# Kernel optimization log

Measured on AMD Instinct MI355X. Metric: run time of the kernel, lower is better.

## Reference

```python
import jax, jax.numpy as jnp
import numpy as np

N_TOKENS = 65536   # number of embeddings to quantize
CODE_DIM = 768     # embedding dim
NUM_CODES = 4096   # codebook size


def setup_inputs() -> dict:
    key = jax.random.key(0)
    k1, k2 = jax.random.split(key)
    x = jax.random.normal(k1, (N_TOKENS, CODE_DIM), dtype=jnp.float32)
    codebook = jax.random.normal(k2, (NUM_CODES, CODE_DIM), dtype=jnp.float32)
    return {"x": x, "codebook": codebook}


def reference(x, codebook):
    # argmin over squared distances == argmin over cdist (sqrt is monotone).
    x2 = jnp.sum(x * x, axis=-1, keepdims=True)          # [N, 1]
    c2 = jnp.sum(codebook * codebook, axis=-1)           # [K]
    dist = x2 + c2[None, :] - 2.0 * jnp.einsum('nd,kd->nk', x, codebook)  # [N, K]
    indices = jnp.argmin(dist, axis=-1)                  # [N] int
    quantized = codebook[indices]                        # gather [N, D]
    # straight-through estimator: forward = quantized, grad flows to x
    q_ste = x + jax.lax.stop_gradient(quantized - x)
    return q_ste, indices
```

## Files before the change

kernel.cpp:

```cpp
#include <hip/hip_runtime.h>

#define N_TOKENS  65536
#define CODE_DIM  768
#define NUM_CODES 4096

#define MARGIN 0.006f
#define FLTMAX 3.4028235e38f

typedef __attribute__((ext_vector_type(8))) short bf16x8;
typedef __attribute__((ext_vector_type(4))) float f32x4;

__device__ __forceinline__ unsigned short f2bf(float f) {
  unsigned int u = __float_as_uint(f);
  unsigned int r = (u + 0x7fffu + ((u >> 16) & 1u)) >> 16;
  return (unsigned short)r;
}
__device__ __forceinline__ float bf2f(unsigned short h) {
  return __uint_as_float(((unsigned int)h) << 16);
}
__device__ __forceinline__ void gl2lds16(const void* g, void* l) {
  __builtin_amdgcn_global_load_lds(
      (const __attribute__((address_space(1))) unsigned int*)g,
      (__attribute__((address_space(3))) unsigned int*)l, 16, 0, 0);
}

__global__ __launch_bounds__(256) void vq_convert_kernel(
    const float* __restrict__ x, const float* __restrict__ cb,
    unsigned short* __restrict__ xh, unsigned short* __restrict__ xl,
    unsigned short* __restrict__ cbh, unsigned short* __restrict__ cbl,
    float* __restrict__ x2, float* __restrict__ c2, int* __restrict__ fcnt) {
  if (blockIdx.x == 0 && threadIdx.x == 0) *fcnt = 0;
  const int wave = threadIdx.x >> 6;
  const int lane = threadIdx.x & 63;
  const int row  = blockIdx.x * 4 + wave;
  const float* src;
  unsigned short *hdst, *ldst;
  float* ndst;
  if (row < N_TOKENS) {
    src = x + (size_t)row * CODE_DIM;
    hdst = xh + (size_t)row * CODE_DIM;
    ldst = xl + (size_t)row * CODE_DIM;
    ndst = x2 + row;
  } else {
    const int r = row - N_TOKENS;
    if (r >= NUM_CODES) return;
    src = cb + (size_t)r * CODE_DIM;
    hdst = cbh + (size_t)r * CODE_DIM;
    ldst = cbl + (size_t)r * CODE_DIM;
    ndst = c2 + r;
  }
  const float4* s4 = (const float4*)src;
  ushort4* h4 = (ushort4*)hdst;
  ushort4* l4 = (ushort4*)ldst;
  float acc = 0.f;
#pragma unroll
  for (int i = 0; i < 3; ++i) {
    float4 f = s4[lane + 64 * i];
    ushort4 h, l;
    h.x = f2bf(f.x); l.x = f2bf(f.x - bf2f(h.x));
    h.y = f2bf(f.y); l.y = f2bf(f.y - bf2f(h.y));
    h.z = f2bf(f.z); l.z = f2bf(f.z - bf2f(h.z));
    h.w = f2bf(f.w); l.w = f2bf(f.w - bf2f(h.w));
    h4[lane + 64 * i] = h;
    l4[lane + 64 * i] = l;
    acc += (f.x * f.x + f.y * f.y) + (f.z * f.z + f.w * f.w);
  }
#pragma unroll
  for (int off = 32; off > 0; off >>= 1) acc += __shfl_down(acc, off, 64);
  if (lane == 0) *ndst = acc;
}

#define BT 256
#define KTILE 256
#define NKT (NUM_CODES / KTILE)
#define NSTEP (CODE_DIM / 32)
#define TOTSTEP (NKT * NSTEP)

__global__ __launch_bounds__(512, 2) void vq_mfma_kernel(
    const unsigned short* __restrict__ xh, const unsigned short* __restrict__ xl,
    const unsigned short* __restrict__ cbh, const unsigned short* __restrict__ cbl,
    const float* __restrict__ c2, const float* __restrict__ cb,
    float* __restrict__ out, int* __restrict__ out_idx,
    int* __restrict__ fcnt, int* __restrict__ flist) {
  __shared__ __align__(16) unsigned short sA[2][BT * 64];
  __shared__ __align__(16) unsigned short sB[2][KTILE * 64];
  __shared__ float redv[512], redsv[512];
  __shared__ int   redi[512];
  __shared__ int   sIdx[256];

  const int tid = threadIdx.x;
  const int wave = tid >> 6, lane = tid & 63;
  const int l15 = lane & 15, quad = lane >> 4;
  const int wr = wave >> 1, wc = wave & 1;
  const int tokBase = blockIdx.x * BT;

  const int lr = lane >> 3;
  const int cc = (lane & 7) ^ lr;
  const int hsel = cc >> 2;
  const int coff = (cc & 3) * 8;
  const unsigned short* pAsrc = hsel ? xl : xh;
  const unsigned short* pBsrc = hsel ? cbl : cbh;
  const size_t aOff = (size_t)(tokBase + wave * 32 + lr) * CODE_DIM + coff;
  const size_t bOff = (size_t)(wave * 32 + lr) * CODE_DIM + coff;

  const int aposh = (quad ^ (l15 & 7)) * 8;
  const int aBaseH = (wr * 64 + l15) * 64 + aposh;
  const int aBaseL = (wr * 64 + l15) * 64 + (aposh ^ 32);
  const int bBaseH = (wc * 128 + l15) * 64 + aposh;
  const int bBaseL = (wc * 128 + l15) * 64 + (aposh ^ 32);

  float v[4][4], sv[4][4];
  int bi[4][4];
#pragma unroll
  for (int i = 0; i < 4; ++i)
#pragma unroll
    for (int r = 0; r < 4; ++r) { v[i][r] = FLTMAX; sv[i][r] = FLTMAX; bi[i][r] = 0; }

  {
#pragma unroll
    for (int t = 0; t < 4; ++t)
      gl2lds16(pAsrc + aOff + (size_t)t * (8 * CODE_DIM),
               &sA[0][(wave * 32 + t * 8) * 64]);
#pragma unroll
    for (int t = 0; t < 4; ++t)
      gl2lds16(pBsrc + bOff + (size_t)t * (8 * CODE_DIM),
               &sB[0][(wave * 32 + t * 8) * 64]);
  }
  asm volatile("s_waitcnt vmcnt(0)" ::: "memory");
  __builtin_amdgcn_s_barrier();
  __builtin_amdgcn_sched_barrier(0);

  for (int kt = 0; kt < NKT; ++kt) {
    f32x4 acc[4][8];
#pragma unroll
    for (int i = 0; i < 4; ++i)
#pragma unroll
      for (int j = 0; j < 8; ++j) acc[i][j] = (f32x4){0.f, 0.f, 0.f, 0.f};

    for (int ksq = 0; ksq < NSTEP; ++ksq) {
      const int gstep = kt * NSTEP + ksq;
      const int cur = gstep & 1;
      const bool more = (gstep < TOTSTEP - 1);
      const int ns = gstep + 1;
      const int nk0 = (ns % NSTEP) * 32;
      const size_t nbb = (size_t)(ns / NSTEP) * (KTILE * (size_t)CODE_DIM);
      const unsigned short* As = sA[cur];
      const unsigned short* Bs = sB[cur];

      if (more) {
#pragma unroll
        for (int t = 0; t < 4; ++t)
          gl2lds16(pAsrc + aOff + (size_t)t * (8 * CODE_DIM) + nk0,
                   &sA[cur ^ 1][(wave * 32 + t * 8) * 64]);
      }

      bf16x8 fah[4], fal[4], fbh[8], fbl[8];
#pragma unroll
      for (int i = 0; i < 4; ++i) fah[i] = *(const bf16x8*)(As + aBaseH + i * 1024);
#pragma unroll
      for (int j = 0; j < 8; ++j) fbh[j] = *(const bf16x8*)(Bs + bBaseH + j * 1024);
      __builtin_amdgcn_s_setprio(1);
#pragma unroll
      for (int i = 0; i < 4; ++i)
#pragma unroll
        for (int j = 0; j < 8; ++j)
          acc[i][j] = __builtin_amdgcn_mfma_f32_16x16x32_bf16(fah[i], fbh[j], acc[i][j], 0, 0, 0);
      __builtin_amdgcn_s_setprio(0);

      if (more) {
#pragma unroll
        for (int t = 0; t < 4; ++t)
          gl2lds16(pBsrc + nbb + bOff + (size_t)t * (8 * CODE_DIM) + nk0,
                   &sB[cur ^ 1][(wave * 32 + t * 8) * 64]);
      }

#pragma unroll
      for (int j = 0; j < 8; ++j) fbl[j] = *(const bf16x8*)(Bs + bBaseL + j * 1024);
      __builtin_amdgcn_s_setprio(1);
#pragma unroll
      for (int i = 0; i < 4; ++i)
#pragma unroll
        for (int j = 0; j < 8; ++j)
          acc[i][j] = __builtin_amdgcn_mfma_f32_16x16x32_bf16(fah[i], fbl[j], acc[i][j], 0, 0, 0);
      __builtin_amdgcn_s_setprio(0);

#pragma unroll
      for (int i = 0; i < 4; ++i) fal[i] = *(const bf16x8*)(As + aBaseL + i * 1024);
      __builtin_amdgcn_s_setprio(1);
#pragma unroll
      for (int i = 0; i < 4; ++i)
#pragma unroll
        for (int j = 0; j < 8; ++j)
          acc[i][j] = __builtin_amdgcn_mfma_f32_16x16x32_bf16(fal[i], fbh[j], acc[i][j], 0, 0, 0);
      __builtin_amdgcn_s_setprio(0);

      asm volatile("s_waitcnt vmcnt(0)" ::: "memory");
      __builtin_amdgcn_s_barrier();
      __builtin_amdgcn_sched_barrier(0);
    }

    const int kbase = kt * KTILE;
#pragma unroll
    for (int j = 0; j < 8; ++j) {
      const int kcol = kbase + wc * 128 + j * 16 + l15;
      const float c2j = c2[kcol];
#pragma unroll
      for (int i = 0; i < 4; ++i)
#pragma unroll
        for (int r = 0; r < 4; ++r) {
          float s = fmaf(-2.0f, acc[i][j][r], c2j);
          float vo = v[i][r];
          sv[i][r] = fminf(sv[i][r], fmaxf(s, vo));
          bool lt = s < vo;
          v[i][r]  = lt ? s : vo;
          bi[i][r] = lt ? kcol : bi[i][r];
        }
    }
  }

#pragma unroll
  for (int i = 0; i < 4; ++i)
#pragma unroll
    for (int r = 0; r < 4; ++r) {
      float vv = v[i][r], svv = sv[i][r];
      int ii = bi[i][r];
#pragma unroll
      for (int m = 1; m < 16; m <<= 1) {
        float ov = __shfl_xor(vv, m, 64);
        float osv = __shfl_xor(svv, m, 64);
        int oi = __shfl_xor(ii, m, 64);
        float nsv = fminf(fminf(svv, osv), fmaxf(vv, ov));
        bool take = (ov < vv) || (ov == vv && oi < ii);
        vv = take ? ov : vv;
        ii = take ? oi : ii;
        svv = nsv;
      }
      if (l15 == 0) {
        int row = wr * 64 + i * 16 + quad * 4 + r;
        redv[row * 2 + wc] = vv;
        redsv[row * 2 + wc] = svv;
        redi[row * 2 + wc] = ii;
      }
    }
  __syncthreads();
  if (tid < 256) {
    float v0 = redv[tid * 2], v1 = redv[tid * 2 + 1];
    float s0 = redsv[tid * 2], s1 = redsv[tid * 2 + 1];
    int i0 = redi[tid * 2], i1 = redi[tid * 2 + 1];
    bool take = (v1 < v0) || (v1 == v0 && i1 < i0);
    float bv = take ? v1 : v0;
    int bidx = take ? i1 : i0;
    float bsv = fminf(fminf(s0, s1), fmaxf(v0, v1));
    out_idx[tokBase + tid] = bidx;
    sIdx[tid] = bidx;
    if (bsv - bv < MARGIN) {
      int p = atomicAdd(fcnt, 1);
      flist[p] = tokBase + tid;
    }
  }
  __syncthreads();
  for (int tt = 0; tt < 32; ++tt) {
    const int t = wave * 32 + tt;
    const int k = sIdx[t];
    const float4* src = (const float4*)(cb + (size_t)k * CODE_DIM);
    float4* dst = (float4*)(out + (size_t)(tokBase + t) * CODE_DIM);
#pragma unroll
    for (int i2 = 0; i2 < 3; ++i2) dst[lane + 64 * i2] = src[lane + 64 * i2];
  }
  if (tid < 256)
    out[(size_t)N_TOKENS * CODE_DIM + tokBase + tid] = (float)sIdx[tid];
}

__global__ __launch_bounds__(256) void vq_rescan_kernel(
    const float* __restrict__ x, const float* __restrict__ cb,
    const float* __restrict__ x2, const float* __restrict__ c2,
    const int* __restrict__ fcnt, const int* __restrict__ flist,
    int* __restrict__ out_idx, float* __restrict__ out) {
  __shared__ float xs[4][CODE_DIM];
  __shared__ float rv[256];
  __shared__ int ri[256];
  const int nf = *fcnt;
  const int ngr = (nf + 3) >> 2;
  for (int g = blockIdx.x; g < ngr; g += gridDim.x) {
    const int base = g * 4;
    int tok[4];
#pragma unroll
    for (int t = 0; t < 4; ++t) tok[t] = flist[min(base + t, nf - 1)];
    __syncthreads();
    if (threadIdx.x < 192) {
#pragma unroll
      for (int t = 0; t < 4; ++t)
        ((float4*)xs[t])[threadIdx.x] =
            ((const float4*)(x + (size_t)tok[t] * CODE_DIM))[threadIdx.x];
    }
    __syncthreads();
    float bv[4]; int bidx[4];
#pragma unroll
    for (int t = 0; t < 4; ++t) { bv[t] = FLTMAX; bidx[t] = 0; }
    for (int kk = 0; kk < NUM_CODES / 256; ++kk) {
      const int k = kk * 256 + threadIdx.x;
      const float4* crow = (const float4*)(cb + (size_t)k * CODE_DIM);
      float a0 = 0.f, a1 = 0.f, a2 = 0.f, a3 = 0.f;
      for (int c = 0; c < CODE_DIM / 4; ++c) {
        float4 cv = crow[c];
        float4 x0 = ((float4*)xs[0])[c];
        float4 x1 = ((float4*)xs[1])[c];
        float4 x2v = ((float4*)xs[2])[c];
        float4 x3 = ((float4*)xs[3])[c];
        a0 += (x0.x * cv.x + x0.y * cv.y) + (x0.z * cv.z + x0.w * cv.w);
        a1 += (x1.x * cv.x + x1.y * cv.y) + (x1.z * cv.z + x1.w * cv.w);
        a2 += (x2v.x * cv.x + x2v.y * cv.y) + (x2v.z * cv.z + x2v.w * cv.w);
        a3 += (x3.x * cv.x + x3.y * cv.y) + (x3.z * cv.z + x3.w * cv.w);
      }
      const float c2k = c2[k];
      float d0 = (x2[tok[0]] + c2k) - 2.0f * a0;
      float d1 = (x2[tok[1]] + c2k) - 2.0f * a1;
      float d2 = (x2[tok[2]] + c2k) - 2.0f * a2;
      float d3 = (x2[tok[3]] + c2k) - 2.0f * a3;
      if (d0 < bv[0]) { bv[0] = d0; bidx[0] = k; }
      if (d1 < bv[1]) { bv[1] = d1; bidx[1] = k; }
      if (d2 < bv[2]) { bv[2] = d2; bidx[2] = k; }
      if (d3 < bv[3]) { bv[3] = d3; bidx[3] = k; }
    }
#pragma unroll
    for (int t = 0; t < 4; ++t) {
      __syncthreads();
      rv[threadIdx.x] = bv[t];
      ri[threadIdx.x] = bidx[t];
      __syncthreads();
      for (int s = 128; s > 0; s >>= 1) {
        if (threadIdx.x < s) {
          float ov = rv[threadIdx.x + s];
          int oi = ri[threadIdx.x + s];
          if (ov < rv[threadIdx.x] ||
              (ov == rv[threadIdx.x] && oi < ri[threadIdx.x])) {
            rv[threadIdx.x] = ov;
            ri[threadIdx.x] = oi;
          }
        }
        __syncthreads();
      }
      const int kfix = ri[0];
      if (base + t < nf) {
        if (threadIdx.x < 192)
          ((float4*)(out + (size_t)tok[t] * CODE_DIM))[threadIdx.x] =
              ((const float4*)(cb + (size_t)kfix * CODE_DIM))[threadIdx.x];
        if (threadIdx.x == 0) {
          out_idx[tok[t]] = kfix;
          out[(size_t)N_TOKENS * CODE_DIM + tok[t]] = (float)kfix;
        }
      }
    }
  }
}

__global__ __launch_bounds__(256) void vq_gather_kernel(
    const float* __restrict__ cb, const int* __restrict__ idx,
    float* __restrict__ out) {
  const int wave = threadIdx.x >> 6;
  const int lane = threadIdx.x & 63;
  const int token = blockIdx.x * 4 + wave;
  const int k = idx[token];
  const float4* src = (const float4*)(cb + (size_t)k * CODE_DIM);
  float4* dst = (float4*)(out + (size_t)token * CODE_DIM);
#pragma unroll
  for (int i = 0; i < 3; ++i) dst[lane + 64 * i] = src[lane + 64 * i];
  if (lane == 0) out[(size_t)N_TOKENS * CODE_DIM + token] = (float)k;
}

#define MT 64
#define KT 128
#define DT 32
#define LDSTRIDE 36

__global__ __launch_bounds__(256) void vq_norms_kernel(
    const float* __restrict__ x, const float* __restrict__ cb,
    float* __restrict__ x2, float* __restrict__ c2) {
  const int wave = threadIdx.x >> 6;
  const int lane = threadIdx.x & 63;
  const int row = blockIdx.x * 4 + wave;
  const float* src;
  float* dst;
  if (row < N_TOKENS) {
    src = x + (size_t)row * CODE_DIM;
    dst = x2 + row;
  } else {
    const int r = row - N_TOKENS;
    if (r >= NUM_CODES) return;
    src = cb + (size_t)r * CODE_DIM;
    dst = c2 + r;
  }
  const float4* s4 = (const float4*)src;
  float acc = 0.f;
#pragma unroll
  for (int i = 0; i < 3; ++i) {
    float4 vv = s4[lane + 64 * i];
    acc += (vv.x * vv.x + vv.y * vv.y) + (vv.z * vv.z + vv.w * vv.w);
  }
#pragma unroll
  for (int off = 32; off > 0; off >>= 1) acc += __shfl_down(acc, off, 64);
  if (lane == 0) *dst = acc;
}

__global__ __launch_bounds__(256) void vq_argmin_kernel(
    const float* __restrict__ x, const float* __restrict__ cb,
    const float* __restrict__ x2, const float* __restrict__ c2,
    int* __restrict__ out_idx) {
  __shared__ float xs[MT * LDSTRIDE];
  __shared__ float cs[KT * LDSTRIDE];
  __shared__ float x2s[MT];
  __shared__ float c2s[KT];
  const int tid = threadIdx.x;
  const int tx = tid & 15;
  const int ty = tid >> 4;
  const int tokBase = blockIdx.x * MT;
  if (tid < MT) x2s[tid] = x2[tokBase + tid];
  float bestv[4];
  int besti[4];
#pragma unroll
  for (int i = 0; i < 4; ++i) { bestv[i] = FLTMAX; besti[i] = 0; }
  const float4* xg = (const float4*)x;
  const float4* cg = (const float4*)cb;
  for (int kt = 0; kt < NUM_CODES / KT; ++kt) {
    const int kBase = kt * KT;
    __syncthreads();
    if (tid < KT) c2s[tid] = c2[kBase + tid];
    float acc[4][8];
#pragma unroll
    for (int i = 0; i < 4; ++i)
#pragma unroll
      for (int j = 0; j < 8; ++j) acc[i][j] = 0.f;
    for (int dc = 0; dc < CODE_DIM / DT; ++dc) {
      __syncthreads();
#pragma unroll
      for (int r = 0; r < 2; ++r) {
        int fidx = tid + 256 * r;
        int row = fidx >> 3, c4 = fidx & 7;
        float4 vv = xg[(size_t)(tokBase + row) * (CODE_DIM / 4) + dc * 8 + c4];
        *(float4*)&xs[row * LDSTRIDE + c4 * 4] = vv;
      }
#pragma unroll
      for (int r = 0; r < 4; ++r) {
        int fidx = tid + 256 * r;
        int row = fidx >> 3, c4 = fidx & 7;
        float4 vv = cg[(size_t)(kBase + row) * (CODE_DIM / 4) + dc * 8 + c4];
        *(float4*)&cs[row * LDSTRIDE + c4 * 4] = vv;
      }
      __syncthreads();
#pragma unroll
      for (int dd = 0; dd < DT / 4; ++dd) {
        float4 xv[4], cv[8];
#pragma unroll
        for (int i = 0; i < 4; ++i)
          xv[i] = *(const float4*)&xs[(ty + 16 * i) * LDSTRIDE + dd * 4];
#pragma unroll
        for (int j = 0; j < 8; ++j)
          cv[j] = *(const float4*)&cs[(tx + 16 * j) * LDSTRIDE + dd * 4];
#pragma unroll
        for (int i = 0; i < 4; ++i)
#pragma unroll
          for (int j = 0; j < 8; ++j)
            acc[i][j] += (xv[i].x * cv[j].x + xv[i].y * cv[j].y) +
                         (xv[i].z * cv[j].z + xv[i].w * cv[j].w);
      }
    }
#pragma unroll
    for (int i = 0; i < 4; ++i) {
      const float xx = x2s[ty + 16 * i];
#pragma unroll
      for (int j = 0; j < 8; ++j) {
        float dist = (xx + c2s[tx + 16 * j]) - 2.0f * acc[i][j];
        int k = kBase + tx + 16 * j;
        if (dist < bestv[i]) { bestv[i] = dist; besti[i] = k; }
      }
    }
  }
  __syncthreads();
  float* rdv = xs;
  int* rdi = (int*)cs;
#pragma unroll
  for (int i = 0; i < 4; ++i) {
    const int m = ty + 16 * i;
    rdv[m * 16 + tx] = bestv[i];
    rdi[m * 16 + tx] = besti[i];
  }
  __syncthreads();
  if (tid < MT) {
    float bv = rdv[tid * 16];
    int bidx = rdi[tid * 16];
#pragma unroll
    for (int t = 1; t < 16; ++t) {
      float vv = rdv[tid * 16 + t];
      int kk = rdi[tid * 16 + t];
      if (vv < bv || (vv == bv && kk < bidx)) { bv = vv; bidx = kk; }
    }
    out_idx[tokBase + tid] = bidx;
  }
}

extern "C" void kernel_launch(void* const* d_in, const int* in_sizes, int n_in,
                              void* d_out, int out_size, void* d_ws, size_t ws_size,
                              hipStream_t stream) {
  (void)in_sizes; (void)n_in; (void)out_size;
  const float* x = (const float*)d_in[0];
  const float* cb = (const float*)d_in[1];
  float* out = (float*)d_out;

  char* w = (char*)d_ws;
  unsigned short* xh = (unsigned short*)w;  w += (size_t)N_TOKENS * CODE_DIM * 2;
  unsigned short* xl = (unsigned short*)w;  w += (size_t)N_TOKENS * CODE_DIM * 2;
  unsigned short* cbh = (unsigned short*)w; w += (size_t)NUM_CODES * CODE_DIM * 2;
  unsigned short* cbl = (unsigned short*)w; w += (size_t)NUM_CODES * CODE_DIM * 2;
  float* x2 = (float*)w;  w += (size_t)N_TOKENS * 4;
  float* c2 = (float*)w;  w += (size_t)NUM_CODES * 4;
  int* idx = (int*)w;     w += (size_t)N_TOKENS * 4;
  int* flist = (int*)w;   w += (size_t)N_TOKENS * 4;
  int* fcnt = (int*)w;    w += 256;
  const size_t need = (size_t)(w - (char*)d_ws);

  if (ws_size >= need) {
    vq_convert_kernel<<<(N_TOKENS + NUM_CODES) / 4, 256, 0, stream>>>(
        x, cb, xh, xl, cbh, cbl, x2, c2, fcnt);
    vq_mfma_kernel<<<N_TOKENS / BT, 512, 0, stream>>>(
        xh, xl, cbh, cbl, c2, cb, out, idx, fcnt, flist);
    vq_rescan_kernel<<<512, 256, 0, stream>>>(x, cb, x2, c2, fcnt, flist, idx, out);
  } else {
    float* fx2 = (float*)d_ws;
    float* fc2 = fx2 + N_TOKENS;
    int* fidx = (int*)(fc2 + NUM_CODES);
    vq_norms_kernel<<<(N_TOKENS + NUM_CODES + 3) / 4, 256, 0, stream>>>(x, cb, fx2, fc2);
    vq_argmin_kernel<<<N_TOKENS / MT, 256, 0, stream>>>(x, cb, fx2, fc2, fidx);
    vq_gather_kernel<<<N_TOKENS / 4, 256, 0, stream>>>(cb, fidx, out);
  }
}
```

Baseline: 1.934 ms.

## Shrink MFMA block tile to 128x128 and move gather to separate kernel

Halves the token and codebook tile sizes, so each block runs 256 threads (4 waves) with a 4x4 MFMA accumulator tile instead of 8 waves with 4x8, and launches twice as many blocks. The codebook-row gather and index-as-float output move out of the MFMA and rescan kernels into the existing standalone gather kernel, which runs after the rescan. LDS fragment loads for the next step are now issued before the global-to-LDS prefetch. The smaller tile lowers per-block LDS and register use and should help occupancy, but it reduces operand reuse per byte loaded and adds another kernel launch.

New measurement: 2.178 ms. 1.13x slower.

```diff
diff --git a/kernel.cpp b/kernel.cpp
--- a/kernel.cpp
+++ b/kernel.cpp
@@ -70,23 +70,21 @@
   if (lane == 0) *ndst = acc;
 }
 
-#define BT 256
-#define KTILE 256
+#define BT 128
+#define KTILE 128
 #define NKT (NUM_CODES / KTILE)
 #define NSTEP (CODE_DIM / 32)
 #define TOTSTEP (NKT * NSTEP)
 
-__global__ __launch_bounds__(512, 2) void vq_mfma_kernel(
+__global__ __launch_bounds__(256, 2) void vq_mfma_kernel(
     const unsigned short* __restrict__ xh, const unsigned short* __restrict__ xl,
     const unsigned short* __restrict__ cbh, const unsigned short* __restrict__ cbl,
-    const float* __restrict__ c2, const float* __restrict__ cb,
-    float* __restrict__ out, int* __restrict__ out_idx,
+    const float* __restrict__ c2, int* __restrict__ out_idx,
     int* __restrict__ fcnt, int* __restrict__ flist) {
   __shared__ __align__(16) unsigned short sA[2][BT * 64];
   __shared__ __align__(16) unsigned short sB[2][KTILE * 64];
-  __shared__ float redv[512], redsv[512];
-  __shared__ int   redi[512];
-  __shared__ int   sIdx[256];
+  __shared__ float redv[256], redsv[256];
+  __shared__ int   redi[256];
 
   const int tid = threadIdx.x;
   const int wave = tid >> 6, lane = tid & 63;
@@ -106,8 +104,8 @@
   const int aposh = (quad ^ (l15 & 7)) * 8;
   const int aBaseH = (wr * 64 + l15) * 64 + aposh;
   const int aBaseL = (wr * 64 + l15) * 64 + (aposh ^ 32);
-  const int bBaseH = (wc * 128 + l15) * 64 + aposh;
-  const int bBaseL = (wc * 128 + l15) * 64 + (aposh ^ 32);
+  const int bBaseH = (wc * 64 + l15) * 64 + aposh;
+  const int bBaseL = (wc * 64 + l15) * 64 + (aposh ^ 32);
 
   float v[4][4], sv[4][4];
   int bi[4][4];
@@ -131,11 +129,11 @@
   __builtin_amdgcn_sched_barrier(0);
 
   for (int kt = 0; kt < NKT; ++kt) {
-    f32x4 acc[4][8];
+    f32x4 acc[4][4];
 #pragma unroll
     for (int i = 0; i < 4; ++i)
 #pragma unroll
-      for (int j = 0; j < 8; ++j) acc[i][j] = (f32x4){0.f, 0.f, 0.f, 0.f};
+      for (int j = 0; j < 4; ++j) acc[i][j] = (f32x4){0.f, 0.f, 0.f, 0.f};
 
     for (int ksq = 0; ksq < NSTEP; ++ksq) {
       const int gstep = kt * NSTEP + ksq;
@@ -147,6 +145,12 @@
       const unsigned short* As = sA[cur];
       const unsigned short* Bs = sB[cur];
 
+      bf16x8 fah[4], fal[4], fbh[4], fbl[4];
+#pragma unroll
+      for (int i = 0; i < 4; ++i) fah[i] = *(const bf16x8*)(As + aBaseH + i * 1024);
+#pragma unroll
+      for (int j = 0; j < 4; ++j) fbh[j] = *(const bf16x8*)(Bs + bBaseH + j * 1024);
+
       if (more) {
 #pragma unroll
         for (int t = 0; t < 4; ++t)
@@ -154,16 +158,11 @@
                    &sA[cur ^ 1][(wave * 32 + t * 8) * 64]);
       }
 
-      bf16x8 fah[4], fal[4], fbh[8], fbl[8];
-#pragma unroll
-      for (int i = 0; i < 4; ++i) fah[i] = *(const bf16x8*)(As + aBaseH + i * 1024);
-#pragma unroll
-      for (int j = 0; j < 8; ++j) fbh[j] = *(const bf16x8*)(Bs + bBaseH + j * 1024);
       __builtin_amdgcn_s_setprio(1);
 #pragma unroll
       for (int i = 0; i < 4; ++i)
 #pragma unroll
-        for (int j = 0; j < 8; ++j)
+        for (int j = 0; j < 4; ++j)
           acc[i][j] = __builtin_amdgcn_mfma_f32_16x16x32_bf16(fah[i], fbh[j], acc[i][j], 0, 0, 0);
       __builtin_amdgcn_s_setprio(0);
 
@@ -175,12 +174,12 @@
       }
 
 #pragma unroll
-      for (int j = 0; j < 8; ++j) fbl[j] = *(const bf16x8*)(Bs + bBaseL + j * 1024);
+      for (int j = 0; j < 4; ++j) fbl[j] = *(const bf16x8*)(Bs + bBaseL + j * 1024);
       __builtin_amdgcn_s_setprio(1);
 #pragma unroll
       for (int i = 0; i < 4; ++i)
 #pragma unroll
-        for (int j = 0; j < 8; ++j)
+        for (int j = 0; j < 4; ++j)
           acc[i][j] = __builtin_amdgcn_mfma_f32_16x16x32_bf16(fah[i], fbl[j], acc[i][j], 0, 0, 0);
       __builtin_amdgcn_s_setprio(0);
 
@@ -190,7 +189,7 @@
 #pragma unroll
       for (int i = 0; i < 4; ++i)
 #pragma unroll
-        for (int j = 0; j < 8; ++j)
+        for (int j = 0; j < 4; ++j)
           acc[i][j] = __builtin_amdgcn_mfma_f32_16x16x32_bf16(fal[i], fbh[j], acc[i][j], 0, 0, 0);
       __builtin_amdgcn_s_setprio(0);
 
@@ -201,8 +200,8 @@
 
     const int kbase = kt * KTILE;
 #pragma unroll
-    for (int j = 0; j < 8; ++j) {
-      const int kcol = kbase + wc * 128 + j * 16 + l15;
+    for (int j = 0; j < 4; ++j) {
+      const int kcol = kbase + wc * 64 + j * 16 + l15;
       const float c2j = c2[kcol];
 #pragma unroll
       for (int i = 0; i < 4; ++i)
@@ -243,7 +242,7 @@
       }
     }
   __syncthreads();
-  if (tid < 256) {
+  if (tid < 128) {
     float v0 = redv[tid * 2], v1 = redv[tid * 2 + 1];
     float s0 = redsv[tid * 2], s1 = redsv[tid * 2 + 1];
     int i0 = redi[tid * 2], i1 = redi[tid * 2 + 1];
@@ -252,30 +251,18 @@
     int bidx = take ? i1 : i0;
     float bsv = fminf(fminf(s0, s1), fmaxf(v0, v1));
     out_idx[tokBase + tid] = bidx;
-    sIdx[tid] = bidx;
     if (bsv - bv < MARGIN) {
       int p = atomicAdd(fcnt, 1);
       flist[p] = tokBase + tid;
     }
   }
-  __syncthreads();
-  for (int tt = 0; tt < 32; ++tt) {
-    const int t = wave * 32 + tt;
-    const int k = sIdx[t];
-    const float4* src = (const float4*)(cb + (size_t)k * CODE_DIM);
-    float4* dst = (float4*)(out + (size_t)(tokBase + t) * CODE_DIM);
-#pragma unroll
-    for (int i2 = 0; i2 < 3; ++i2) dst[lane + 64 * i2] = src[lane + 64 * i2];
-  }
-  if (tid < 256)
-    out[(size_t)N_TOKENS * CODE_DIM + tokBase + tid] = (float)sIdx[tid];
 }
 
 __global__ __launch_bounds__(256) void vq_rescan_kernel(
     const float* __restrict__ x, const float* __restrict__ cb,
     const float* __restrict__ x2, const float* __restrict__ c2,
     const int* __restrict__ fcnt, const int* __restrict__ flist,
-    int* __restrict__ out_idx, float* __restrict__ out) {
+    int* __restrict__ out_idx) {
   __shared__ float xs[4][CODE_DIM];
   __shared__ float rv[256];
   __shared__ int ri[256];
@@ -340,16 +327,7 @@
         }
         __syncthreads();
       }
-      const int kfix = ri[0];
-      if (base + t < nf) {
-        if (threadIdx.x < 192)
-          ((float4*)(out + (size_t)tok[t] * CODE_DIM))[threadIdx.x] =
-              ((const float4*)(cb + (size_t)kfix * CODE_DIM))[threadIdx.x];
-        if (threadIdx.x == 0) {
-          out_idx[tok[t]] = kfix;
-          out[(size_t)N_TOKENS * CODE_DIM + tok[t]] = (float)kfix;
-        }
-      }
+      if (threadIdx.x == 0 && base + t < nf) out_idx[tok[t]] = ri[0];
     }
   }
 }
@@ -521,9 +499,10 @@
   if (ws_size >= need) {
     vq_convert_kernel<<<(N_TOKENS + NUM_CODES) / 4, 256, 0, stream>>>(
         x, cb, xh, xl, cbh, cbl, x2, c2, fcnt);
-    vq_mfma_kernel<<<N_TOKENS / BT, 512, 0, stream>>>(
-        xh, xl, cbh, cbl, c2, cb, out, idx, fcnt, flist);
-    vq_rescan_kernel<<<512, 256, 0, stream>>>(x, cb, x2, c2, fcnt, flist, idx, out);
+    vq_mfma_kernel<<<N_TOKENS / BT, 256, 0, stream>>>(
+        xh, xl, cbh, cbl, c2, idx, fcnt, flist);
+    vq_rescan_kernel<<<512, 256, 0, stream>>>(x, cb, x2, c2, fcnt, flist, idx);
+    vq_gather_kernel<<<N_TOKENS / 4, 256, 0, stream>>>(cb, idx, out);
   } else {
     float* fx2 = (float*)d_ws;
     float* fc2 = fx2 + N_TOKENS;
```
